# Optimization experiments

Measured on AMD Instinct MI355X. Metric: run time of the kernel, lower is better.

The kernel has to match this reference:

```python
import jax, jax.numpy as jnp
import numpy as np

N = 50000       # nodes
E = 800000      # edges
IN_DIM = 256    # input_dim
HEADS = 4
CH = 32         # per-head channels (hidden_dim; conv3 uses latent_dim//heads = 32 too)
HC = HEADS * CH # 128
ED = 32         # edge_dims


def setup_inputs():
    key = jax.random.key(0)
    ks = iter(jax.random.split(key, 64))
    def nrm(shape):
        return jax.random.normal(next(ks), shape, dtype=jnp.float32) * 0.05
    inp = {}
    inp["x"] = nrm((N, IN_DIM))
    inp["edge_index"] = jax.random.randint(next(ks), (2, E), 0, N)
    inp["attr"] = nrm((E, ED))
    for l, ind in ((1, IN_DIM), (2, HC), (3, HC)):
        inp[f"Wq{l}"] = nrm((ind, HC)); inp[f"bq{l}"] = jnp.zeros((HC,), jnp.float32)
        inp[f"Wk{l}"] = nrm((ind, HC)); inp[f"bk{l}"] = jnp.zeros((HC,), jnp.float32)
        inp[f"Wv{l}"] = nrm((ind, HC)); inp[f"bv{l}"] = jnp.zeros((HC,), jnp.float32)
        inp[f"We{l}"] = nrm((ED, HC))  # lin_edge has no bias in PyG TransformerConv
        inp[f"Ws{l}"] = nrm((ind, HC)); inp[f"bs{l}"] = jnp.zeros((HC,), jnp.float32)
    inp["g1"] = jnp.ones((HC,), jnp.float32); inp["be1"] = jnp.zeros((HC,), jnp.float32)
    inp["g2"] = jnp.ones((HC,), jnp.float32); inp["be2"] = jnp.zeros((HC,), jnp.float32)
    return inp


def _transformer_conv(x, src, dst, attr, Wq, bq, Wk, bk, Wv, bv, We, Ws, bs):
    # PyG TransformerConv, concat=True, root_weight=True, beta=False, dropout=0 (eval).
    q = (x @ Wq + bq).reshape(-1, HEADS, CH)   # [N,H,C] (queries at dst)
    k = (x @ Wk + bk).reshape(-1, HEADS, CH)
    v = (x @ Wv + bv).reshape(-1, HEADS, CH)
    e = (attr @ We).reshape(-1, HEADS, CH)     # [E,H,C]
    kj = k[src] + e                            # edge-conditioned keys  [E,H,C]
    vj = v[src] + e                            # edge-conditioned values [E,H,C]
    alpha = jnp.einsum('ehc,ehc->eh', q[dst], kj) / np.sqrt(CH).astype(np.float32)
    # segment softmax over incoming edges per destination node, per head
    amax = jax.ops.segment_max(alpha, dst, num_segments=N)          # [N,H]
    amax = jnp.where(jnp.isfinite(amax), amax, 0.0)                 # nodes with no edges
    ex = jnp.exp(alpha - amax[dst])                                 # [E,H]
    den = jax.ops.segment_sum(ex, dst, num_segments=N)              # [N,H]
    a = ex / (den[dst] + 1e-16)                                     # [E,H]
    out = jax.ops.segment_sum(a[..., None] * vj, dst, num_segments=N)  # [N,H,C]
    out = out.reshape(-1, HC) + (x @ Ws + bs)                       # + root skip
    return out, a


def _layernorm(x, g, b):
    m = x.mean(-1, keepdims=True)
    v = x.var(-1, keepdims=True)
    return (x - m) / jnp.sqrt(v + 1e-5) * g + b


def reference(x, edge_index, attr,
              Wq1, bq1, Wk1, bk1, Wv1, bv1, We1, Ws1, bs1,
              Wq2, bq2, Wk2, bk2, Wv2, bv2, We2, Ws2, bs2,
              Wq3, bq3, Wk3, bk3, Wv3, bv3, We3, Ws3, bs3,
              g1, be1, g2, be2):
    src, dst = edge_index[0], edge_index[1]
    h, a1 = _transformer_conv(x, src, dst, attr, Wq1, bq1, Wk1, bk1, Wv1, bv1, We1, Ws1, bs1)
    h = jax.nn.relu(_layernorm(h, g1, be1))   # dropout is identity in eval
    h, a2 = _transformer_conv(h, src, dst, attr, Wq2, bq2, Wk2, bk2, Wv2, bv2, We2, Ws2, bs2)
    h = jax.nn.relu(_layernorm(h, g2, be2))
    h, a3 = _transformer_conv(h, src, dst, attr, Wq3, bq3, Wk3, bk3, Wv3, bv3, We3, Ws3, bs3)
    return (h, a1, a2, a3)
```

## Files before the change

kernel.cpp:

```cpp
#include <hip/hip_runtime.h>
#include <math.h>

#define N_NODES 50000
#define E_EDGES 800000
#define HC 128
#define ED 32

typedef __attribute__((ext_vector_type(8))) short bf16x8;
typedef __attribute__((ext_vector_type(4))) float f32x4;
typedef unsigned short ushort_t;

__device__ __forceinline__ ushort_t f2bf(float f){
    unsigned u = __float_as_uint(f);
    return (ushort_t)((u + 0x7FFFu + ((u >> 16) & 1u)) >> 16);
}
__device__ __forceinline__ float bflo(unsigned u){ return __uint_as_float(u << 16); }
__device__ __forceinline__ float bfhi(unsigned u){ return __uint_as_float(u & 0xffff0000u); }

__device__ __forceinline__ int weidx(int c, int d){
    return c * 40 + (((((d >> 2) + ((c >> 3) & 7)) & 7)) << 2) + (d & 3);
}


__global__ void hist_kernel(const int* __restrict__ dst, int* __restrict__ cnt, int n_edges){
    int e = blockIdx.x * blockDim.x + threadIdx.x;
    if (e < n_edges) atomicAdd(&cnt[dst[e]], 1);
}

__global__ __launch_bounds__(1024) void scan_sort_kernel(
    const int* __restrict__ cnt, int* __restrict__ rowptr,
    int* __restrict__ cursor, int* __restrict__ norder)
{
    __shared__ int part[1024];
    __shared__ int wbins[1024];
    __shared__ int wcur[1024];
    __shared__ int binbase[64];
    const int t = threadIdx.x;
    const int wave = t >> 6;
    const int CH = (N_NODES + 1023) / 1024;
    const int base = t * CH;
    int s = 0;
    for (int i = 0; i < CH; i++){
        int idx = base + i;
        if (idx < N_NODES) s += cnt[idx];
    }
    part[t] = s;
    wbins[t] = 0;
    __syncthreads();
    for (int off = 1; off < 1024; off <<= 1){
        int v = (t >= off) ? part[t - off] : 0;
        __syncthreads();
        part[t] += v;
        __syncthreads();
    }
    int off = (t == 0) ? 0 : part[t - 1];
    for (int i = 0; i < CH; i++){
        int idx = base + i;
        if (idx < N_NODES){
            int c = cnt[idx];
            rowptr[idx] = off;
            cursor[idx] = off;
            off += c;
        }
    }
    if (t == 1023) rowptr[N_NODES] = part[1023];
    __syncthreads();

    for (int i = t; i < N_NODES; i += 1024){
        int d = cnt[i]; if (d > 63) d = 63;
        atomicAdd(&wbins[(wave << 6) + d], 1);
    }
    __syncthreads();
    if (t < 64){
        int tot = 0;
        #pragma unroll
        for (int w = 0; w < 16; w++) tot += wbins[(w << 6) + t];
        binbase[t] = tot;
    }
    __syncthreads();
    if (t == 0){
        int acc = 0;
        for (int b = 0; b < 64; b++){ int c = binbase[b]; binbase[b] = acc; acc += c; }
    }
    __syncthreads();
    {
        int b = t & 63, w = t >> 6;
        int acc = binbase[b];
        for (int w2 = 0; w2 < w; w2++) acc += wbins[(w2 << 6) + b];
        wcur[t] = acc;
    }
    __syncthreads();
    for (int i = t; i < N_NODES; i += 1024){
        int d = cnt[i]; if (d > 63) d = 63;
        int pos = atomicAdd(&wcur[(wave << 6) + d], 1);
        norder[pos] = i;
    }
}

__global__ void scatter_kernel(const int* __restrict__ src, const int* __restrict__ dst,
                               int* __restrict__ cursor, int2* __restrict__ es, int n_edges){
    int e = blockIdx.x * blockDim.x + threadIdx.x;
    if (e < n_edges){
        int d = dst[e];
        int pos = atomicAdd(&cursor[d], 1);
        es[pos] = make_int2(e, src[e]);
    }
}

__device__ __forceinline__ void pack_item(const float* __restrict__ Wq, const float* __restrict__ Wk,
                                          const float* __restrict__ Wv, const float* __restrict__ Ws,
                                          const float* __restrict__ We, ushort_t* __restrict__ Bp,
                                          int K, int item){
    int n = item % 640, k = item / 640;
    float val;
    if (n < 512){
        const float* W = (n < 128) ? Wq : (n < 256) ? Wk : (n < 384) ? Wv : Ws;
        val = W[k * HC + (n & 127)];
    } else {
        int col = n - 512, h5 = (col >> 5) * 32, d = col & 31;
        float acc = 0.f;
        for (int c = 0; c < 32; c++)
            acc = fmaf(Wq[k * HC + h5 + c], We[d * HC + h5 + c], acc);
        val = acc;
    }
    Bp[(((size_t)(k >> 3)) * 640 + n) * 8 + (k & 7)] = f2bf(val);
}

#define T_S0 12800000
#define T_S1 16000000
#define T_S2 16163840
#define T_S3 16245760
#define T_S4 16327680
#define T_S5 16328064

__global__ __launch_bounds__(256) void tail_kernel(
    const float* __restrict__ attr, const int2* __restrict__ es,
    const float* __restrict__ x, int perm_mode,
    ushort_t* __restrict__ attr_bf, ushort_t* __restrict__ Xbf,
    const float* __restrict__ Wq0, const float* __restrict__ bq0, const float* __restrict__ Wk0,
    const float* __restrict__ Wv0, const float* __restrict__ Ws0, const float* __restrict__ We0,
    const float* __restrict__ Wq1, const float* __restrict__ bq1, const float* __restrict__ Wk1,
    const float* __restrict__ Wv1, const float* __restrict__ Ws1, const float* __restrict__ We1,
    const float* __restrict__ Wq2, const float* __restrict__ bq2, const float* __restrict__ Wk2,
    const float* __restrict__ Wv2, const float* __restrict__ Ws2, const float* __restrict__ We2,
    ushort_t* __restrict__ Bp0, ushort_t* __restrict__ Bp1, ushort_t* __restrict__ Bp2,
    float* __restrict__ qwb3)
{
    const int stride = gridDim.x * blockDim.x;
    for (int gi = blockIdx.x * blockDim.x + threadIdx.x; gi < T_S5; gi += stride){
        if (gi < T_S0){
            if (perm_mode){
                int grp = gi >> 4, lane = gi & 15;
                int e = es[grp].x;
                const float2 v = *(const float2*)&attr[(size_t)e * ED + lane * 2];
                unsigned r = (unsigned)f2bf(v.x) | ((unsigned)f2bf(v.y) << 16);
                ((unsigned*)attr_bf)[(size_t)grp * (ED / 2) + lane] = r;
            }
        } else if (gi < T_S1){
            int i = gi - T_S0;
            float4 v = ((const float4*)x)[i];
            ushort_t r0 = f2bf(v.x), r1 = f2bf(v.y), r2 = f2bf(v.z), r3 = f2bf(v.w);
            ((ushort4*)Xbf)[i] = make_ushort4(r0, r1, r2, r3);
        } else if (gi < T_S2){
            pack_item(Wq0, Wk0, Wv0, Ws0, We0, Bp0, 256, gi - T_S1);
        } else if (gi < T_S3){
            pack_item(Wq1, Wk1, Wv1, Ws1, We1, Bp1, 128, gi - T_S2);
        } else if (gi < T_S4){
            pack_item(Wq2, Wk2, Wv2, Ws2, We2, Bp2, 128, gi - T_S3);
        } else {
            int f = gi - T_S4;
            int l = f >> 7, t2 = f & 127;
            const float* bq = (l == 0) ? bq0 : (l == 1) ? bq1 : bq2;
            const float* We = (l == 0) ? We0 : (l == 1) ? We1 : We2;
            int h5 = (t2 >> 5) * 32, d = t2 & 31;
            float acc = 0.f;
            for (int c = 0; c < 32; c++)
                acc = fmaf(bq[h5 + c], We[d * HC + h5 + c], acc);
            qwb3[l * HC + t2] = acc;
        }
    }
}

template<int K>
__global__ __launch_bounds__(320) void gemm_mfma(
    const ushort_t* __restrict__ Xbf, const ushort_t* __restrict__ Bpack,
    const float* __restrict__ b0, const float* __restrict__ b1,
    const float* __restrict__ b2, const float* __restrict__ b3,
    const float* __restrict__ b4,
    float* __restrict__ Yq, ushort_t* __restrict__ Ykbf,
    ushort_t* __restrict__ Yvbf, float* __restrict__ Ys,
    float* __restrict__ Yw, int M)
{
    const int w = threadIdx.x >> 6;
    const int lane = threadIdx.x & 63;
    const int q = lane >> 4, nn = lane & 15;
    const int row0 = blockIdx.x * 32;

    f32x4 acc[2][8];
    #pragma unroll
    for (int mt = 0; mt < 2; mt++)
        #pragma unroll
        for (int nt = 0; nt < 8; nt++)
            acc[mt][nt] = (f32x4){0.f, 0.f, 0.f, 0.f};

    const int r0 = row0 + nn;
    const int r1 = row0 + 16 + nn;
    const bf16x8 zf = (bf16x8){0,0,0,0,0,0,0,0};

    #pragma unroll
    for (int kc = 0; kc < K / 32; kc++){
        bf16x8 a0 = (r0 < M) ? *(const bf16x8*)&Xbf[(size_t)r0 * K + kc * 32 + q * 8] : zf;
        bf16x8 a1 = (r1 < M) ? *(const bf16x8*)&Xbf[(size_t)r1 * K + kc * 32 + q * 8] : zf;
        bf16x8 b[8];
        #pragma unroll
        for (int nt = 0; nt < 8; nt++){
            int n = w * 128 + nt * 16 + nn;
            b[nt] = *(const bf16x8*)&Bpack[(((size_t)(kc * 4 + q)) * 640 + n) * 8];
        }
        #pragma unroll
        for (int nt = 0; nt < 8; nt++){
            acc[0][nt] = __builtin_amdgcn_mfma_f32_16x16x32_bf16(a0, b[nt], acc[0][nt], 0, 0, 0);
            acc[1][nt] = __builtin_amdgcn_mfma_f32_16x16x32_bf16(a1, b[nt], acc[1][nt], 0, 0, 0);
        }
    }

    const float scale = (w == 0 || w == 4) ? 0.17677669529663687f : 1.f;
    const float* bias = (w == 0) ? b0 : (w == 1) ? b1 : (w == 2) ? b2 : (w == 3) ? b3 : b4;

    if (w == 1 || w == 2){
        ushort_t* Yb = (w == 1) ? Ykbf : Yvbf;
        #pragma unroll
        for (int nt = 0; nt < 8; nt++){
            int col = nt * 16 + nn;
            float bval = bias[col];
            #pragma unroll
            for (int mt = 0; mt < 2; mt++){
                #pragma unroll
                for (int r = 0; r < 4; r++){
                    int row = row0 + mt * 16 + q * 4 + r;
                    if (row < M) Yb[(size_t)row * HC + col] = f2bf(acc[mt][nt][r] + bval);
                }
            }
        }
    } else {
        float* Y = (w == 0) ? Yq : (w == 3) ? Ys : Yw;
        #pragma unroll
        for (int nt = 0; nt < 8; nt++){
            int col = nt * 16 + nn;
            float bval = bias[col];
            #pragma unroll
            for (int mt = 0; mt < 2; mt++){
                #pragma unroll
                for (int r = 0; r < 4; r++){
                    int row = row0 + mt * 16 + q * 4 + r;
                    if (row < M) Y[(size_t)row * HC + col] = (acc[mt][nt][r] + bval) * scale;
                }
            }
        }
    }
}

__device__ __forceinline__ float dot16s(const uint4 kk, const uint4 aa,
                                        const float4 qA, const float4 qB,
                                        const float4 wA, const float4 wB){
    float pa =            bflo(kk.x) * qA.x;
    pa = fmaf(bfhi(kk.x), qA.y, pa);
    pa = fmaf(bflo(kk.y), qA.z, pa);
    pa = fmaf(bfhi(kk.y), qA.w, pa);
    pa = fmaf(bflo(aa.x), wA.x, pa);
    pa = fmaf(bfhi(aa.x), wA.y, pa);
    pa = fmaf(bflo(aa.y), wA.z, pa);
    pa = fmaf(bfhi(aa.y), wA.w, pa);
    float pb =            bflo(kk.z) * qB.x;
    pb = fmaf(bfhi(kk.z), qB.y, pb);
    pb = fmaf(bflo(kk.w), qB.z, pb);
    pb = fmaf(bfhi(kk.w), qB.w, pb);
    pb = fmaf(bflo(aa.z), wB.x, pb);
    pb = fmaf(bfhi(aa.z), wB.y, pb);
    pb = fmaf(bflo(aa.w), wB.z, pb);
    pb = fmaf(bfhi(aa.w), wB.w, pb);
    return pa + pb;
}

__device__ __forceinline__ uint4 packrow(const float* p){
    float4 x = *(const float4*)p;
    float4 y = *(const float4*)(p + 4);
    uint4 r;
    r.x = (unsigned)f2bf(x.x) | ((unsigned)f2bf(x.y) << 16);
    r.y = (unsigned)f2bf(x.z) | ((unsigned)f2bf(x.w) << 16);
    r.z = (unsigned)f2bf(y.x) | ((unsigned)f2bf(y.y) << 16);
    r.w = (unsigned)f2bf(y.z) | ((unsigned)f2bf(y.w) << 16);
    return r;
}

__global__ __launch_bounds__(256) void fused_attn_kernel(
    const float* __restrict__ qs, const float* __restrict__ qw,
    const ushort_t* __restrict__ kb, const ushort_t* __restrict__ vb,
    const float* __restrict__ skip, const float* __restrict__ We,
    const float* __restrict__ attr, const ushort_t* __restrict__ attr_bf, int perm_mode,
    const int* __restrict__ rowptr, const int2* __restrict__ es,
    const int* __restrict__ norder,
    float* __restrict__ acsr, float* __restrict__ a_out,
    const float* __restrict__ g, const float* __restrict__ be,
    float* __restrict__ out_f32, ushort_t* __restrict__ out_bf, int apply_ln)
{
    __shared__ float WeT[5120];
    __shared__ float SL[2304];
    const int t = threadIdx.x;
    for (int idx = t; idx < ED * HC; idx += 256){
        int d = idx >> 7, c = idx & 127;
        WeT[weidx(c, d)] = We[idx];
    }
    __syncthreads();

    const int lane = t & 63, wvi = t >> 6;
    const int qq = lane >> 4, li = lane & 15;
    const int h = li >> 2, jj = li & 3;
    const int gq = blockIdx.x * 16 + wvi * 4 + qq;
    if (gq >= N_NODES) return;
    const int n = norder[gq];
    const int ch = h * 32 + jj * 8;
    const size_t nrow = (size_t)n * HC + ch;

    const float4 qA = *(const float4*)&qs[nrow];
    const float4 qB = *(const float4*)&qs[nrow + 4];
    const float4 wA = *(const float4*)&qw[nrow];
    const float4 wB = *(const float4*)&qw[nrow + 4];
    const float4 skA = *(const float4*)&skip[nrow];
    const float4 skB = *(const float4*)&skip[nrow + 4];

    const int beg = rowptr[n], end = rowptr[n + 1];
    float m = -1e30f, s = 0.f;
    float acc[8] = {0,0,0,0,0,0,0,0};
    float S[8]   = {0,0,0,0,0,0,0,0};

    for (int i = beg; i < end; i += 4){
        const int cnt = end - i;
        uint4 kk[4], vv[4], aa[4];
        #pragma unroll
        for (int b = 0; b < 4; b++){
            kk[b] = (uint4){0,0,0,0}; vv[b] = (uint4){0,0,0,0}; aa[b] = (uint4){0,0,0,0};
            if (b < cnt){
                const int2 e = es[i + b];
                kk[b] = *(const uint4*)&kb[(size_t)e.y * HC + ch];
                vv[b] = *(const uint4*)&vb[(size_t)e.y * HC + ch];
                if (perm_mode)
                    aa[b] = *(const uint4*)&attr_bf[(size_t)(i + b) * ED + jj * 8];
                else
                    aa[b] = packrow(&attr[(size_t)e.x * ED + jj * 8]);
            }
        }
        float al[4];
        #pragma unroll
        for (int b = 0; b < 4; b++){
            float p = dot16s(kk[b], aa[b], qA, qB, wA, wB);
            p += __shfl_xor(p, 1);
            p += __shfl_xor(p, 2);
            al[b] = (b < cnt) ? p : -1e38f;
        }
        if (jj == 0){
            #pragma unroll
            for (int b = 0; b < 4; b++)
                if (b < cnt) acsr[(size_t)(i + b) * 4 + h] = al[b];
        }
        const float mn = fmaxf(fmaxf(m, fmaxf(al[0], al[1])), fmaxf(al[2], al[3]));
        const float sc = __expf(m - mn);
        m = mn;
        const float w0 = __expf(al[0] - mn);
        const float w1 = __expf(al[1] - mn);
        const float w2 = __expf(al[2] - mn);
        const float w3 = __expf(al[3] - mn);
        s = fmaf(s, sc, (w0 + w1) + (w2 + w3));
        acc[0] = fmaf(acc[0], sc, fmaf(w0, bflo(vv[0].x), fmaf(w1, bflo(vv[1].x), fmaf(w2, bflo(vv[2].x), w3 * bflo(vv[3].x)))));
        acc[1] = fmaf(acc[1], sc, fmaf(w0, bfhi(vv[0].x), fmaf(w1, bfhi(vv[1].x), fmaf(w2, bfhi(vv[2].x), w3 * bfhi(vv[3].x)))));
        acc[2] = fmaf(acc[2], sc, fmaf(w0, bflo(vv[0].y), fmaf(w1, bflo(vv[1].y), fmaf(w2, bflo(vv[2].y), w3 * bflo(vv[3].y)))));
        acc[3] = fmaf(acc[3], sc, fmaf(w0, bfhi(vv[0].y), fmaf(w1, bfhi(vv[1].y), fmaf(w2, bfhi(vv[2].y), w3 * bfhi(vv[3].y)))));
        acc[4] = fmaf(acc[4], sc, fmaf(w0, bflo(vv[0].z), fmaf(w1, bflo(vv[1].z), fmaf(w2, bflo(vv[2].z), w3 * bflo(vv[3].z)))));
        acc[5] = fmaf(acc[5], sc, fmaf(w0, bfhi(vv[0].z), fmaf(w1, bfhi(vv[1].z), fmaf(w2, bfhi(vv[2].z), w3 * bfhi(vv[3].z)))));
        acc[6] = fmaf(acc[6], sc, fmaf(w0, bflo(vv[0].w), fmaf(w1, bflo(vv[1].w), fmaf(w2, bflo(vv[2].w), w3 * bflo(vv[3].w)))));
        acc[7] = fmaf(acc[7], sc, fmaf(w0, bfhi(vv[0].w), fmaf(w1, bfhi(vv[1].w), fmaf(w2, bfhi(vv[2].w), w3 * bfhi(vv[3].w)))));
        S[0] = fmaf(S[0], sc, fmaf(w0, bflo(aa[0].x), fmaf(w1, bflo(aa[1].x), fmaf(w2, bflo(aa[2].x), w3 * bflo(aa[3].x)))));
        S[1] = fmaf(S[1], sc, fmaf(w0, bfhi(aa[0].x), fmaf(w1, bfhi(aa[1].x), fmaf(w2, bfhi(aa[2].x), w3 * bfhi(aa[3].x)))));
        S[2] = fmaf(S[2], sc, fmaf(w0, bflo(aa[0].y), fmaf(w1, bflo(aa[1].y), fmaf(w2, bflo(aa[2].y), w3 * bflo(aa[3].y)))));
        S[3] = fmaf(S[3], sc, fmaf(w0, bfhi(aa[0].y), fmaf(w1, bfhi(aa[1].y), fmaf(w2, bfhi(aa[2].y), w3 * bfhi(aa[3].y)))));
        S[4] = fmaf(S[4], sc, fmaf(w0, bflo(aa[0].z), fmaf(w1, bflo(aa[1].z), fmaf(w2, bflo(aa[2].z), w3 * bflo(aa[3].z)))));
        S[5] = fmaf(S[5], sc, fmaf(w0, bfhi(aa[0].z), fmaf(w1, bfhi(aa[1].z), fmaf(w2, bfhi(aa[2].z), w3 * bfhi(aa[3].z)))));
        S[6] = fmaf(S[6], sc, fmaf(w0, bflo(aa[0].w), fmaf(w1, bflo(aa[1].w), fmaf(w2, bflo(aa[2].w), w3 * bflo(aa[3].w)))));
        S[7] = fmaf(S[7], sc, fmaf(w0, bfhi(aa[0].w), fmaf(w1, bfhi(aa[1].w), fmaf(w2, bfhi(aa[2].w), w3 * bfhi(aa[3].w)))));
    }

    const int nl = wvi * 4 + qq;
    const int sbase = nl * 144;
    const int hsk = h * 36;
    *(float4*)&SL[sbase + hsk + jj * 8]     = make_float4(S[0], S[1], S[2], S[3]);
    *(float4*)&SL[sbase + hsk + jj * 8 + 4] = make_float4(S[4], S[5], S[6], S[7]);
    asm volatile("" ::: "memory");
    float E[8] = {0,0,0,0,0,0,0,0};
    #pragma unroll
    for (int d4 = 0; d4 < 8; d4++){
        const float4 sv = *(const float4*)&SL[sbase + hsk + d4 * 4];
        #pragma unroll
        for (int r = 0; r < 8; r++){
            const float4 wv = *(const float4*)&WeT[weidx(ch + r, d4 * 4)];
            E[r] = fmaf(sv.x, wv.x, fmaf(sv.y, wv.y, fmaf(sv.z, wv.z, fmaf(sv.w, wv.w, E[r]))));
        }
    }

    const float inv = 1.f / (s + 1e-16f);
    float o[8];
    o[0] = (acc[0] + E[0]) * inv + skA.x;
    o[1] = (acc[1] + E[1]) * inv + skA.y;
    o[2] = (acc[2] + E[2]) * inv + skA.z;
    o[3] = (acc[3] + E[3]) * inv + skA.w;
    o[4] = (acc[4] + E[4]) * inv + skB.x;
    o[5] = (acc[5] + E[5]) * inv + skB.y;
    o[6] = (acc[6] + E[6]) * inv + skB.z;
    o[7] = (acc[7] + E[7]) * inv + skB.w;

    if (apply_ln){
        float s1 = 0.f, s2 = 0.f;
        #pragma unroll
        for (int r = 0; r < 8; r++){ s1 += o[r]; s2 = fmaf(o[r], o[r], s2); }
        #pragma unroll
        for (int off = 1; off <= 8; off <<= 1){
            s1 += __shfl_xor(s1, off);
            s2 += __shfl_xor(s2, off);
        }
        const float mu  = s1 * (1.f / 128.f);
        const float var = s2 * (1.f / 128.f) - mu * mu;
        const float ivs = rsqrtf(var + 1e-5f);
        const float4 gA = *(const float4*)&g[ch];
        const float4 gB = *(const float4*)&g[ch + 4];
        const float4 bA = *(const float4*)&be[ch];
        const float4 bB = *(const float4*)&be[ch + 4];
        o[0] = fmaxf((o[0] - mu) * ivs * gA.x + bA.x, 0.f);
        o[1] = fmaxf((o[1] - mu) * ivs * gA.y + bA.y, 0.f);
        o[2] = fmaxf((o[2] - mu) * ivs * gA.z + bA.z, 0.f);
        o[3] = fmaxf((o[3] - mu) * ivs * gA.w + bA.w, 0.f);
        o[4] = fmaxf((o[4] - mu) * ivs * gB.x + bB.x, 0.f);
        o[5] = fmaxf((o[5] - mu) * ivs * gB.y + bB.y, 0.f);
        o[6] = fmaxf((o[6] - mu) * ivs * gB.z + bB.z, 0.f);
        o[7] = fmaxf((o[7] - mu) * ivs * gB.w + bB.w, 0.f);
        uint4 st;
        st.x = (unsigned)f2bf(o[0]) | ((unsigned)f2bf(o[1]) << 16);
        st.y = (unsigned)f2bf(o[2]) | ((unsigned)f2bf(o[3]) << 16);
        st.z = (unsigned)f2bf(o[4]) | ((unsigned)f2bf(o[5]) << 16);
        st.w = (unsigned)f2bf(o[6]) | ((unsigned)f2bf(o[7]) << 16);
        *(uint4*)&out_bf[nrow] = st;
    } else {
        *(float4*)&out_f32[nrow]     = make_float4(o[0], o[1], o[2], o[3]);
        *(float4*)&out_f32[nrow + 4] = make_float4(o[4], o[5], o[6], o[7]);
    }

    const float mh = __shfl(m, (qq << 4) + ((li & 3) << 2));
    const float dh = __shfl(s, (qq << 4) + ((li & 3) << 2));
    const float ih = 1.f / (dh + 1e-16f);
    asm volatile("s_waitcnt vmcnt(0)" ::: "memory");
    for (int f = beg * 4 + li; f < end * 4; f += 16){
        const int e = es[f >> 2].x;
        a_out[(size_t)e * 4 + (li & 3)] = __expf(acsr[f] - mh) * ih;
    }
}


extern "C" void kernel_launch(void* const* d_in, const int* in_sizes, int n_in,
                              void* d_out, int out_size, void* d_ws, size_t ws_size,
                              hipStream_t stream) {
    const float* x    = (const float*)d_in[0];
    const int*   ei   = (const int*)  d_in[1];
    const float* attr = (const float*)d_in[2];
    const float* gln[2]  = { (const float*)d_in[30], (const float*)d_in[32] };
    const float* beln[2] = { (const float*)d_in[31], (const float*)d_in[33] };

    float* out   = (float*)d_out;
    float* h_out = out;
    float* a_out[3] = { out + (size_t)N_NODES * HC,
                        out + (size_t)N_NODES * HC + (size_t)E_EDGES * 4,
                        out + (size_t)N_NODES * HC + (size_t)2 * E_EDGES * 4 };

    char* base = (char*)d_ws;
    size_t off = 0;
    auto alloc = [&](size_t bytes) -> void* {
        void* p = base + off;
        off = (off + bytes + 63) & ~(size_t)63;
        return p;
    };
    const size_t NB = (size_t)N_NODES * HC;
    float* qbuf     = (float*)alloc(NB * 4);
    float* qwbuf    = (float*)alloc(NB * 4);
    ushort_t* kbf   = (ushort_t*)alloc(NB * 2);
    ushort_t* vbf   = (ushort_t*)alloc(NB * 2);
    float* sbuf     = (float*)alloc(NB * 4);
    int* rowptr     = (int*)alloc((N_NODES + 1) * 4);
    int* cnt        = (int*)alloc(N_NODES * 4);
    int* cursor     = (int*)alloc(N_NODES * 4);
    int* norder     = (int*)alloc(N_NODES * 4);
    int2* es        = (int2*)alloc((size_t)E_EDGES * 8);
    ushort_t* Xbf   = (ushort_t*)alloc((size_t)N_NODES * 256 * 2);
    ushort_t* Hbf   = (ushort_t*)alloc(NB * 2);
    ushort_t* Bp0   = (ushort_t*)alloc((size_t)256 * 640 * 2);
    ushort_t* Bp1   = (ushort_t*)alloc((size_t)128 * 640 * 2);
    ushort_t* Bp2   = (ushort_t*)alloc((size_t)128 * 640 * 2);
    float* acsr     = (float*)alloc((size_t)E_EDGES * 4 * 4);
    float* qwb3     = (float*)alloc((size_t)3 * HC * 4);
    ushort_t* attr_bf = (ushort_t*)alloc((size_t)E_EDGES * ED * 2);
    const int perm_mode = (ws_size >= off) ? 1 : 0;

    const int* srcp = ei;
    const int* dstp = ei + E_EDGES;

    hipMemsetAsync(cnt, 0, (size_t)N_NODES * 4, stream);
    hist_kernel<<<(E_EDGES + 255) / 256, 256, 0, stream>>>(dstp, cnt, E_EDGES);
    scan_sort_kernel<<<1, 1024, 0, stream>>>(cnt, rowptr, cursor, norder);
    scatter_kernel<<<(E_EDGES + 255) / 256, 256, 0, stream>>>(srcp, dstp, cursor, es, E_EDGES);
    tail_kernel<<<4096, 256, 0, stream>>>(
        attr, es, x, perm_mode, attr_bf, Xbf,
        (const float*)d_in[3],  (const float*)d_in[4],  (const float*)d_in[5],
        (const float*)d_in[7],  (const float*)d_in[10], (const float*)d_in[9],
        (const float*)d_in[12], (const float*)d_in[13], (const float*)d_in[14],
        (const float*)d_in[16], (const float*)d_in[19], (const float*)d_in[18],
        (const float*)d_in[21], (const float*)d_in[22], (const float*)d_in[23],
        (const float*)d_in[25], (const float*)d_in[28], (const float*)d_in[27],
        Bp0, Bp1, Bp2, qwb3);

    const int gemm_grid = (N_NODES + 31) / 32;
    const int attn_grid = (N_NODES + 15) / 16;
    ushort_t* Bps[3] = { Bp0, Bp1, Bp2 };

    for (int l = 0; l < 3; l++){
        const float* bq = (const float*)d_in[3 + 9 * l + 1];
        const float* bk = (const float*)d_in[3 + 9 * l + 3];
        const float* bv = (const float*)d_in[3 + 9 * l + 5];
        const float* We = (const float*)d_in[3 + 9 * l + 6];
        const float* bs = (const float*)d_in[3 + 9 * l + 8];

        if (l == 0)
            gemm_mfma<256><<<gemm_grid, 320, 0, stream>>>(Xbf, Bps[l], bq, bk, bv, bs, qwb3 + 128 * l,
                                                          qbuf, kbf, vbf, sbuf, qwbuf, N_NODES);
        else
            gemm_mfma<128><<<gemm_grid, 320, 0, stream>>>(Hbf, Bps[l], bq, bk, bv, bs, qwb3 + 128 * l,
                                                          qbuf, kbf, vbf, sbuf, qwbuf, N_NODES);

        const float* gg = (l < 2) ? gln[l] : nullptr;
        const float* bb = (l < 2) ? beln[l] : nullptr;
        fused_attn_kernel<<<attn_grid, 256, 0, stream>>>(
            qbuf, qwbuf, kbf, vbf, sbuf, We, attr, attr_bf, perm_mode,
            rowptr, es, norder, acsr, a_out[l], gg, bb,
            (l < 2) ? nullptr : h_out, (l < 2) ? Hbf : nullptr, (l < 2) ? 1 : 0);
    }
}
```

Before: 1.065 ms.

## Parallelize degree-bucket node ordering across blocks via chunked histograms

Moves the degree-bucket counting sort of nodes out of the single-block scan kernel. A new multi-block kernel builds per-chunk degree histograms, the scan kernel turns them into per-chunk bucket offsets, and the first 64 blocks of the edge scatter kernel place nodes into norder. This cuts the serial single-block work that sits on the critical path, at the cost of one extra kernel launch and extra global traffic for the chunk histograms.

```diff
diff --git a/kernel.cpp b/kernel.cpp
--- a/kernel.cpp
+++ b/kernel.cpp
@@ -5,6 +5,8 @@
 #define E_EDGES 800000
 #define HC 128
 #define ED 32
+#define SCH 64
+#define SCHSZ 782
 
 typedef __attribute__((ext_vector_type(8))) short bf16x8;
 typedef __attribute__((ext_vector_type(4))) float f32x4;
@@ -27,16 +29,30 @@
     if (e < n_edges) atomicAdd(&cnt[dst[e]], 1);
 }
 
+__global__ __launch_bounds__(256) void chunk_hist_kernel(const int* __restrict__ cnt,
+                                                         int* __restrict__ chist){
+    __shared__ int hist[64];
+    const int t = threadIdx.x, b = blockIdx.x;
+    if (t < 64) hist[t] = 0;
+    __syncthreads();
+    const int base = b * SCHSZ;
+    const int lim = min(base + SCHSZ, N_NODES);
+    for (int i = base + t; i < lim; i += 256){
+        int d = cnt[i]; if (d > 63) d = 63;
+        atomicAdd(&hist[d], 1);
+    }
+    __syncthreads();
+    if (t < 64) chist[b * 64 + t] = hist[t];
+}
+
 __global__ __launch_bounds__(1024) void scan_sort_kernel(
     const int* __restrict__ cnt, int* __restrict__ rowptr,
-    int* __restrict__ cursor, int* __restrict__ norder)
+    int* __restrict__ cursor, const int* __restrict__ chist, int* __restrict__ cbase)
 {
     __shared__ int part[1024];
-    __shared__ int wbins[1024];
-    __shared__ int wcur[1024];
+    __shared__ int ch[SCH * 64];
     __shared__ int binbase[64];
     const int t = threadIdx.x;
-    const int wave = t >> 6;
     const int CH = (N_NODES + 1023) / 1024;
     const int base = t * CH;
     int s = 0;
@@ -45,7 +61,6 @@
         if (idx < N_NODES) s += cnt[idx];
     }
     part[t] = s;
-    wbins[t] = 0;
     __syncthreads();
     for (int off = 1; off < 1024; off <<= 1){
         int v = (t >= off) ? part[t - off] : 0;
@@ -64,46 +79,52 @@
         }
     }
     if (t == 1023) rowptr[N_NODES] = part[1023];
-    __syncthreads();
-
-    for (int i = t; i < N_NODES; i += 1024){
-        int d = cnt[i]; if (d > 63) d = 63;
-        atomicAdd(&wbins[(wave << 6) + d], 1);
-    }
+
+    for (int i = t; i < SCH * 64; i += 1024) ch[i] = chist[i];
     __syncthreads();
     if (t < 64){
         int tot = 0;
-        #pragma unroll
-        for (int w = 0; w < 16; w++) tot += wbins[(w << 6) + t];
+        for (int c = 0; c < SCH; c++) tot += ch[c * 64 + t];
         binbase[t] = tot;
     }
     __syncthreads();
     if (t == 0){
         int acc = 0;
-        for (int b = 0; b < 64; b++){ int c = binbase[b]; binbase[b] = acc; acc += c; }
-    }
-    __syncthreads();
-    {
-        int b = t & 63, w = t >> 6;
-        int acc = binbase[b];
-        for (int w2 = 0; w2 < w; w2++) acc += wbins[(w2 << 6) + b];
-        wcur[t] = acc;
-    }
-    __syncthreads();
-    for (int i = t; i < N_NODES; i += 1024){
-        int d = cnt[i]; if (d > 63) d = 63;
-        int pos = atomicAdd(&wcur[(wave << 6) + d], 1);
-        norder[pos] = i;
-    }
-}
-
-__global__ void scatter_kernel(const int* __restrict__ src, const int* __restrict__ dst,
-                               int* __restrict__ cursor, int2* __restrict__ es, int n_edges){
-    int e = blockIdx.x * blockDim.x + threadIdx.x;
+        for (int b = 0; b < 64; b++){ int v = binbase[b]; binbase[b] = acc; acc += v; }
+    }
+    __syncthreads();
+    for (int i = t; i < SCH * 64; i += 1024){
+        int c = i >> 6, d = i & 63;
+        int acc = binbase[d];
+        for (int c2 = 0; c2 < c; c2++) acc += ch[c2 * 64 + d];
+        cbase[i] = acc;
+    }
+}
+
+__global__ __launch_bounds__(256) void scatter_kernel(
+    const int* __restrict__ src, const int* __restrict__ dst,
+    int* __restrict__ cursor, int2* __restrict__ es, int n_edges,
+    const int* __restrict__ cnt, const int* __restrict__ cbase, int* __restrict__ norder)
+{
+    __shared__ int cur[64];
+    const int b = blockIdx.x, t = threadIdx.x;
+    const bool sorter = (b < SCH);
+    if (sorter && t < 64) cur[t] = cbase[b * 64 + t];
+    int e = b * 256 + t;
     if (e < n_edges){
         int d = dst[e];
         int pos = atomicAdd(&cursor[d], 1);
         es[pos] = make_int2(e, src[e]);
+    }
+    if (sorter){
+        __syncthreads();
+        const int base = b * SCHSZ;
+        const int lim = min(base + SCHSZ, N_NODES);
+        for (int i = base + t; i < lim; i += 256){
+            int d = cnt[i]; if (d > 63) d = 63;
+            int pos = atomicAdd(&cur[d], 1);
+            norder[pos] = i;
+        }
     }
 }
 
@@ -495,6 +516,8 @@
     int* cnt        = (int*)alloc(N_NODES * 4);
     int* cursor     = (int*)alloc(N_NODES * 4);
     int* norder     = (int*)alloc(N_NODES * 4);
+    int* chist      = (int*)alloc(SCH * 64 * 4);
+    int* cbase      = (int*)alloc(SCH * 64 * 4);
     int2* es        = (int2*)alloc((size_t)E_EDGES * 8);
     ushort_t* Xbf   = (ushort_t*)alloc((size_t)N_NODES * 256 * 2);
     ushort_t* Hbf   = (ushort_t*)alloc(NB * 2);
@@ -511,8 +534,10 @@
 
     hipMemsetAsync(cnt, 0, (size_t)N_NODES * 4, stream);
     hist_kernel<<<(E_EDGES + 255) / 256, 256, 0, stream>>>(dstp, cnt, E_EDGES);
-    scan_sort_kernel<<<1, 1024, 0, stream>>>(cnt, rowptr, cursor, norder);
-    scatter_kernel<<<(E_EDGES + 255) / 256, 256, 0, stream>>>(srcp, dstp, cursor, es, E_EDGES);
+    chunk_hist_kernel<<<SCH, 256, 0, stream>>>(cnt, chist);
+    scan_sort_kernel<<<1, 1024, 0, stream>>>(cnt, rowptr, cursor, chist, cbase);
+    scatter_kernel<<<(E_EDGES + 255) / 256, 256, 0, stream>>>(
+        srcp, dstp, cursor, es, E_EDGES, cnt, cbase, norder);
     tail_kernel<<<4096, 256, 0, stream>>>(
         attr, es, x, perm_mode, attr_bf, Xbf,
         (const float*)d_in[3],  (const float*)d_in[4],  (const float*)d_in[5],
```

Result: no change. 1.046 ms (-1.8%).
